# Performance work log

Measured on AMD Instinct MI355X. Metric: run time of the kernel, lower is better.

Reference implementation:

```python
import jax, jax.numpy as jnp
import numpy as np

S = 4096      # sequence length
E = 256       # embedding_dim
H = 256       # hidden_dim // 2 (per direction)
T = 16        # tagset size
V = 100000    # vocab size
START = 14
STOP = 15
NEG = -10000.0


def setup_inputs() -> dict:
    key = jax.random.key(0)
    ks = jax.random.split(key, 16)
    trans = jax.random.normal(ks[12], (T, T), jnp.float32)
    trans = trans.at[START, :].set(NEG).at[:, STOP].set(NEG)
    return {
        "sentence": jax.random.randint(ks[0], (S,), 0, V),
        "embed": jax.random.normal(ks[1], (V, E), jnp.float32),
        "W_ih_f": jax.random.normal(ks[2], (4 * H, E), jnp.float32) * 0.05,
        "W_hh_f": jax.random.normal(ks[3], (4 * H, H), jnp.float32) * 0.05,
        "b_ih_f": jax.random.normal(ks[4], (4 * H,), jnp.float32) * 0.05,
        "b_hh_f": jax.random.normal(ks[5], (4 * H,), jnp.float32) * 0.05,
        "W_ih_b": jax.random.normal(ks[6], (4 * H, E), jnp.float32) * 0.05,
        "W_hh_b": jax.random.normal(ks[7], (4 * H, H), jnp.float32) * 0.05,
        "b_ih_b": jax.random.normal(ks[8], (4 * H,), jnp.float32) * 0.05,
        "b_hh_b": jax.random.normal(ks[9], (4 * H,), jnp.float32) * 0.05,
        "W_out": jax.random.normal(ks[10], (T, 2 * H), jnp.float32) * 0.05,
        "b_out": jax.random.normal(ks[11], (T,), jnp.float32) * 0.05,
        "transitions": trans,
        "h0": jax.random.normal(ks[13], (2, H), jnp.float32),
        "c0": jax.random.normal(ks[14], (2, H), jnp.float32),
    }


def _lstm(x, h0, c0, W_ih, W_hh, b_ih, b_hh):
    """Single-direction LSTM over x:[S,E]; PyTorch gate order i,f,g,o."""
    b = b_ih + b_hh
    xg = x @ W_ih.T + b  # [S, 4H] precompute input contribution

    def step(carry, xt):
        h, c = carry
        g = xt + h @ W_hh.T
        i, f, gg, o = jnp.split(g, 4)
        i = jax.nn.sigmoid(i)
        f = jax.nn.sigmoid(f)
        gg = jnp.tanh(gg)
        o = jax.nn.sigmoid(o)
        c = f * c + i * gg
        h = o * jnp.tanh(c)
        return (h, c), h

    _, hs = jax.lax.scan(step, (h0, c0), xg)
    return hs  # [S, H]


def reference(sentence, embed, W_ih_f, W_hh_f, b_ih_f, b_hh_f,
              W_ih_b, W_hh_b, b_ih_b, b_hh_b, W_out, b_out,
              transitions, h0, c0):
    x = embed[sentence]  # [S, E]
    hf = _lstm(x, h0[0], c0[0], W_ih_f, W_hh_f, b_ih_f, b_hh_f)
    hb = _lstm(x[::-1], h0[1], c0[1], W_ih_b, W_hh_b, b_ih_b, b_hh_b)[::-1]
    feats = jnp.concatenate([hf, hb], axis=-1) @ W_out.T + b_out  # [S, T]

    # CRF forward algorithm (log partition). transitions[i, j] = score j -> i.
    alpha0 = jnp.full((T,), NEG, feats.dtype).at[START].set(0.0)

    def crf_step(alpha, emit):
        a = jax.nn.logsumexp(alpha[None, :] + transitions, axis=1) + emit
        return a, None

    alpha, _ = jax.lax.scan(crf_step, alpha0, feats)
    return jax.nn.logsumexp(alpha + transitions[STOP])
```

## Files before the change

kernel.cpp:

```cpp
#include <hip/hip_runtime.h>
#include <hip/hip_bf16.h>

#define S 4096
#define E 256
#define HH 256
#define TT 16
#define NEG_ -10000.0f
#define START_ 14
#define STOP_ 15

__device__ __forceinline__ float fast_exp(float x) {
    return __builtin_amdgcn_exp2f(x * 1.4426950408889634f);
}
__device__ __forceinline__ float fast_log(float x) {
    return 0.6931471805599453f * __builtin_amdgcn_logf(x);
}

__global__ __launch_bounds__(64) void quant4_kernel(
    const float* __restrict__ Wf, const float* __restrict__ Wb,
    const float* __restrict__ h0,
    int* __restrict__ wq4, float* __restrict__ wscale,
    int* __restrict__ hq0p, float* __restrict__ sh0)
{
    int blk = blockIdx.x, lane = threadIdx.x;
    const float* src;
    int* dst;
    float* scl;
    if (blk < 2048) {
        int d = blk >> 10, r = blk & 1023;
        src = (d == 0 ? Wf : Wb) + (size_t)r * 256;
        dst = wq4 + ((size_t)(d * 1024 + r)) * 32;
        scl = wscale + (d * 1024 + r);
    } else {
        int d = blk - 2048;
        src = h0 + (size_t)d * 256;
        dst = hq0p + d * 32;
        scl = sh0 + d;
    }
    float4 a = make_float4(0.f, 0.f, 0.f, 0.f), b = a;
    if (lane < 32) {
        a = ((const float4*)src)[2 * lane];
        b = ((const float4*)src)[2 * lane + 1];
    }
    float f[8] = {a.x, a.y, a.z, a.w, b.x, b.y, b.z, b.w};
    float m = 0.f;
    #pragma unroll
    for (int k = 0; k < 8; ++k) m = fmaxf(m, fabsf(f[k]));
    #pragma unroll
    for (int off = 1; off < 64; off <<= 1) m = fmaxf(m, __shfl_xor(m, off, 64));
    m = fmaxf(m, 1e-20f);
    float inv = 7.0f / m;
    if (lane < 32) {
        int dw = 0;
        #pragma unroll
        for (int k = 0; k < 8; ++k) {
            int q = __float2int_rn(f[k] * inv);
            q = max(-8, min(7, q));
            dw |= (q & 0xF) << (4 * k);
        }
        dst[lane] = dw;
    }
    if (lane == 0) *scl = m / 7.0f;
}

__global__ __launch_bounds__(256) void xg_kernel(
    const int* __restrict__ sent, const float* __restrict__ embed,
    const float* __restrict__ Wf, const float* __restrict__ bihf, const float* __restrict__ bhhf,
    const float* __restrict__ Wb, const float* __restrict__ bihb, const float* __restrict__ bhhb,
    float* __restrict__ xg)
{
    const int dir = blockIdx.y;
    const int t0 = blockIdx.x * 16;
    const int tid = threadIdx.x;
    const float* W = dir ? Wb : Wf;
    __shared__ float xt[16][256];
    for (int tt = 0; tt < 16; ++tt) {
        int t = t0 + tt;
        int pos = dir ? (S - 1 - t) : t;
        int w = sent[pos];
        xt[tt][tid] = embed[(size_t)w * 256 + tid];
    }
    __syncthreads();
    float acc[4][16];
    #pragma unroll
    for (int rc = 0; rc < 4; ++rc)
        #pragma unroll
        for (int tt = 0; tt < 16; ++tt) acc[rc][tt] = 0.f;
    for (int e = 0; e < 256; ++e) {
        float xv[16];
        #pragma unroll
        for (int tt = 0; tt < 16; ++tt) xv[tt] = xt[tt][e];
        #pragma unroll
        for (int rc = 0; rc < 4; ++rc) {
            float w = W[(size_t)(rc * 256 + tid) * 256 + e];
            #pragma unroll
            for (int tt = 0; tt < 16; ++tt) acc[rc][tt] += w * xv[tt];
        }
    }
    const float* bih = dir ? bihb : bihf;
    const float* bhh = dir ? bhhb : bhhf;
    float b0 = bih[0 * 256 + tid] + bhh[0 * 256 + tid];
    float b1 = bih[1 * 256 + tid] + bhh[1 * 256 + tid];
    float b2 = bih[2 * 256 + tid] + bhh[2 * 256 + tid];
    float b3 = bih[3 * 256 + tid] + bhh[3 * 256 + tid];
    #pragma unroll
    for (int tt = 0; tt < 16; ++tt) {
        float4 v;
        v.x = acc[0][tt] + b0;
        v.y = acc[1][tt] + b1;
        v.z = acc[2][tt] + b2;
        v.w = acc[3][tt] + b3;
        ((float4*)(xg + ((size_t)dir * S + (t0 + tt)) * 1024))[tid] = v;
    }
}

#define D8(a,w,h) "v_dot8_i32_i4 " a ", " w ", " h ", " a "\n\t"
#define CHK(h0,h1,h2,h3, a0,a1,a2,a3, b0,b1,b2,b3) \
  D8("v128",a0,h0) D8("v130",b0,h0) D8("v129",a1,h1) D8("v131",b1,h1) \
  D8("v128",a2,h2) D8("v130",b2,h2) D8("v129",a3,h3) D8("v131",b3,h3)

#define LSTM_BODY(XA0, XA1, BPAIR) \
  "global_load_dwordx2 " BPAIR ", v136, %[sxg]\n\t" \
  "ds_read_b128 v[96:99],   v138\n\t" \
  "ds_read_b128 v[100:103], v138 offset:16\n\t" \
  "ds_read_b128 v[104:107], v138 offset:32\n\t" \
  "ds_read_b128 v[108:111], v138 offset:48\n\t" \
  "ds_read_b128 v[112:115], v138 offset:64\n\t" \
  "ds_read_b128 v[116:119], v138 offset:80\n\t" \
  "ds_read_b128 v[120:123], v138 offset:96\n\t" \
  "ds_read_b128 v[124:127], v138 offset:112\n\t" \
  "v_mov_b32 v128, 0\n\t" \
  "v_mov_b32 v129, 0\n\t" \
  "v_mov_b32 v130, 0\n\t" \
  "v_mov_b32 v131, 0\n\t" \
  "s_waitcnt lgkmcnt(6)\n\t" \
  CHK("v96","v97","v98","v99",     "v32","v33","v34","v35", "v64","v65","v66","v67") \
  CHK("v100","v101","v102","v103", "v36","v37","v38","v39", "v68","v69","v70","v71") \
  "s_waitcnt lgkmcnt(4)\n\t" \
  CHK("v104","v105","v106","v107", "v40","v41","v42","v43", "v72","v73","v74","v75") \
  CHK("v108","v109","v110","v111", "v44","v45","v46","v47", "v76","v77","v78","v79") \
  "s_waitcnt lgkmcnt(2)\n\t" \
  CHK("v112","v113","v114","v115", "v48","v49","v50","v51", "v80","v81","v82","v83") \
  CHK("v116","v117","v118","v119", "v52","v53","v54","v55", "v84","v85","v86","v87") \
  "s_waitcnt lgkmcnt(0)\n\t" \
  CHK("v120","v121","v122","v123", "v56","v57","v58","v59", "v88","v89","v90","v91") \
  CHK("v124","v125","v126","v127", "v60","v61","v62","v63", "v92","v93","v94","v95") \
  "v_add_u32 v128, v128, v129\n\t" \
  "v_add_u32 v130, v130, v131\n\t" \
  "v_cvt_f32_i32 v140, v128\n\t" \
  "v_cvt_f32_i32 v141, v130\n\t" \
  "s_waitcnt vmcnt(2)\n\t" \
  "v_fma_f32 v142, v151, v140, " XA0 "\n\t" \
  "v_fma_f32 v143, v152, v141, " XA1 "\n\t" \
  "v_mov_b32 v151, %[s1f]\n\t" \
  "v_mov_b32 v152, %[s2f]\n\t" \
  "v_med3_f32 v142, v142, %[ncl], %[pcl]\n\t" \
  "v_mul_f32 v140, %[kk1], v142\n\t" \
  "v_mul_f32 v144, %[nk], v143\n\t" \
  "v_exp_f32 v140, v140\n\t" \
  "v_exp_f32 v144, v144\n\t" \
  "s_nop 1\n\t" \
  "v_fma_f32 v141, v140, %[mk], %[bk]\n\t" \
  "v_add_f32 v142, 1.0, v140\n\t" \
  "v_add_f32 v145, 1.0, v144\n\t" \
  "v_rcp_f32 v142, v142\n\t" \
  "v_rcp_f32 v145, v145\n\t" \
  "s_nop 1\n\t" \
  "v_mul_f32 v146, v141, v142\n\t" \
  "s_nop 1\n\t" \
  "v_mov_b32_dpp v147, v146 quad_perm:[1,0,3,2] row_mask:0xf bank_mask:0xf\n\t" \
  "v_mov_b32_dpp v148, v145 quad_perm:[1,0,3,2] row_mask:0xf bank_mask:0xf\n\t" \
  "v_cndmask_b32 v140, v146, v147, %[pm]\n\t" \
  "v_cndmask_b32 v141, v145, v148, %[pm]\n\t" \
  "v_cndmask_b32 v142, v147, v146, %[pm]\n\t" \
  "v_cndmask_b32 v143, v148, v145, %[pm]\n\t" \
  "v_mul_f32 v150, v141, v150\n\t" \
  "v_fmac_f32 v150, v140, v142\n\t" \
  "v_med3_f32 v140, v150, %[ncl], %[pcl]\n\t" \
  "v_mul_f32 v140, %[k2], v140\n\t" \
  "v_exp_f32 v140, v140\n\t" \
  "s_nop 1\n\t" \
  "v_add_f32 v141, -1.0, v140\n\t" \
  "v_add_f32 v142, 1.0, v140\n\t" \
  "v_rcp_f32 v142, v142\n\t" \
  "s_nop 1\n\t" \
  "v_mul_f32 v141, v141, v142\n\t" \
  "v_mul_f32 v144, v143, v141\n\t" \
  "global_store_dword v137, v144, %[shs]\n\t" \
  "v_mul_f32 v140, %[c7], v144\n\t" \
  "v_rndne_f32 v140, v140\n\t" \
  "v_cvt_i32_f32 v140, v140\n\t" \
  "v_and_b32 v140, 15, v140\n\t" \
  "s_nop 1\n\t" \
  "v_mov_b32_dpp v141, v140 quad_perm:[2,3,0,1] row_mask:0xf bank_mask:0xf\n\t" \
  "v_lshlrev_b32 v141, 4, v141\n\t" \
  "v_or_b32 v140, v140, v141\n\t" \
  "ds_write_b8 v139, v140\n\t" \
  "v_add_u32 v136, 0x1000, v136\n\t" \
  "v_add_u32 v137, 0x400, v137\n\t" \
  "v_xor_b32 v138, 0x80, v138\n\t" \
  "v_xor_b32 v139, 0x80, v139\n\t" \
  "s_waitcnt lgkmcnt(0)\n\t" \
  "s_barrier\n\t"

__global__ __launch_bounds__(512, 2) void lstm_kernel(
    const float* __restrict__ xg, const int* __restrict__ wq4,
    const float* __restrict__ wscale, const int* __restrict__ hq0p,
    const float* __restrict__ sh0, const float* __restrict__ c0,
    float* __restrict__ hs)
{
    const int d = blockIdx.x;
    const int t = threadIdx.x;
    const int m = t >> 1;
    const int odd = t & 1;
    const int r1 = odd * 512 + m;
    const int r2 = r1 + 256;

    __shared__ alignas(16) int hq4buf[128];

    const int*   wq_d = wq4 + (size_t)d * 32768;
    const float* xg_d = xg + (size_t)d * S * 1024;
    float*       hs_d = hs + (size_t)d * S * 256;
    const float s1 = wscale[d * 1024 + r1];
    const float s2 = wscale[d * 1024 + r2];
    const float sh0v = sh0[d];
    const float c0v = c0[d * 256 + m];
    const int h0v = hq0p[d * 32 + (t & 31)];
    const unsigned h0a  = (unsigned)(t & 31) * 4u;
    const unsigned xoff = (unsigned)t * 8u;
    const unsigned hoff = (unsigned)m * 4u;
    const unsigned voA  = (unsigned)r1 * 128u;
    const unsigned voB  = (unsigned)r2 * 128u;
    const unsigned waddr = ((t & 3) == 0) ? (128u + (unsigned)(t >> 2))
                                          : (256u + (unsigned)(t & 63));
    const float sc1i = s1 * sh0v, sc2i = s2 * sh0v;
    const float sc1f = s1 * (1.0f / 7.0f);
    const float sc2f = s2 * (1.0f / 7.0f);
    const float kk1 = odd ? 2.8853900817779268f : -1.4426950408889634f;
    const float mkv = odd ? 1.0f : 0.0f;
    const float bkv = odd ? -1.0f : 1.0f;
    const float nkv = -1.4426950408889634f;
    const float k2v = 2.8853900817779268f;
    const float c7 = 7.0f;
    const float nclv = -30.0f, pclv = 30.0f;
    const unsigned long long pmask = 0xAAAAAAAAAAAAAAAAULL;
    const unsigned lds_keep = (unsigned)(size_t)&hq4buf[0];
    int cnt = S / 2;

    asm volatile(
        "v_mov_b32 v136, %[xoff]\n\t"
        "v_mov_b32 v137, %[hoff]\n\t"
        "v_mov_b32 v138, 0\n\t"
        "v_mov_b32 v139, %[wad]\n\t"
        "v_mov_b32 v150, %[c0v]\n\t"
        "v_mov_b32 v151, %[s1i]\n\t"
        "v_mov_b32 v152, %[s2i]\n\t"
        "ds_write_b32 %[h0a], %[h0v]\n\t"
        "global_load_dwordx4 v[32:35], %[voA], %[swq]\n\t"
        "global_load_dwordx4 v[36:39], %[voA], %[swq] offset:16\n\t"
        "global_load_dwordx4 v[40:43], %[voA], %[swq] offset:32\n\t"
        "global_load_dwordx4 v[44:47], %[voA], %[swq] offset:48\n\t"
        "global_load_dwordx4 v[48:51], %[voA], %[swq] offset:64\n\t"
        "global_load_dwordx4 v[52:55], %[voA], %[swq] offset:80\n\t"
        "global_load_dwordx4 v[56:59], %[voA], %[swq] offset:96\n\t"
        "global_load_dwordx4 v[60:63], %[voA], %[swq] offset:112\n\t"
        "global_load_dwordx4 v[64:67], %[voB], %[swq]\n\t"
        "global_load_dwordx4 v[68:71], %[voB], %[swq] offset:16\n\t"
        "global_load_dwordx4 v[72:75], %[voB], %[swq] offset:32\n\t"
        "global_load_dwordx4 v[76:79], %[voB], %[swq] offset:48\n\t"
        "global_load_dwordx4 v[80:83], %[voB], %[swq] offset:64\n\t"
        "global_load_dwordx4 v[84:87], %[voB], %[swq] offset:80\n\t"
        "global_load_dwordx4 v[88:91], %[voB], %[swq] offset:96\n\t"
        "global_load_dwordx4 v[92:95], %[voB], %[swq] offset:112\n\t"
        "global_load_dwordx2 v[132:133], v136, %[sxg]\n\t"
        "v_add_u32 v136, 0x1000, v136\n\t"
        "s_waitcnt vmcnt(0) lgkmcnt(0)\n\t"
        "s_barrier\n\t"
        "Llstm%=:\n\t"
        LSTM_BODY("v132", "v133", "v[134:135]")
        LSTM_BODY("v134", "v135", "v[132:133]")
        "s_add_i32 %[cnt], %[cnt], -1\n\t"
        "s_cmp_lg_u32 %[cnt], 0\n\t"
        "s_cbranch_scc1 Llstm%=\n\t"
        : [cnt] "+s"(cnt)
        : [sxg] "s"(xg_d), [shs] "s"(hs_d), [swq] "s"(wq_d), [pm] "s"(pmask),
          [xoff] "v"(xoff), [hoff] "v"(hoff), [wad] "v"(waddr), [c0v] "v"(c0v),
          [s1i] "v"(sc1i), [s2i] "v"(sc2i), [s1f] "v"(sc1f), [s2f] "v"(sc2f),
          [kk1] "v"(kk1), [mk] "v"(mkv), [bk] "v"(bkv), [nk] "v"(nkv),
          [k2] "v"(k2v), [c7] "v"(c7), [ncl] "v"(nclv), [pcl] "v"(pclv),
          [voA] "v"(voA), [voB] "v"(voB), [h0a] "v"(h0a), [h0v] "v"(h0v),
          [keep] "v"(lds_keep)
        : "memory", "scc",
          "v32","v33","v34","v35","v36","v37","v38","v39",
          "v40","v41","v42","v43","v44","v45","v46","v47",
          "v48","v49","v50","v51","v52","v53","v54","v55",
          "v56","v57","v58","v59","v60","v61","v62","v63",
          "v64","v65","v66","v67","v68","v69","v70","v71",
          "v72","v73","v74","v75","v76","v77","v78","v79",
          "v80","v81","v82","v83","v84","v85","v86","v87",
          "v88","v89","v90","v91","v92","v93","v94","v95",
          "v96","v97","v98","v99","v100","v101","v102","v103",
          "v104","v105","v106","v107","v108","v109","v110","v111",
          "v112","v113","v114","v115","v116","v117","v118","v119",
          "v120","v121","v122","v123","v124","v125","v126","v127",
          "v128","v129","v130","v131","v132","v133","v134","v135",
          "v136","v137","v138","v139","v140","v141","v142","v143",
          "v144","v145","v146","v147","v148","v149","v150","v151","v152");
}

__global__ __launch_bounds__(256) void feats_kernel(
    const float* __restrict__ hs, const float* __restrict__ Wout,
    const float* __restrict__ bout, float* __restrict__ feats)
{
    __shared__ float Wl[16][513];
    int tid = threadIdx.x;
    for (int i = tid; i < 16 * 512; i += 256) Wl[i >> 9][i & 511] = Wout[i];
    __syncthreads();
    int tt = tid >> 4, tag = tid & 15;
    int tcur = blockIdx.x * 16 + tt;
    const float* hf = hs + (size_t)tcur * 256;
    const float* hb = hs + (size_t)S * 256 + (size_t)(S - 1 - tcur) * 256;
    float acc = bout[tag];
    for (int k = 0; k < 256; ++k) acc += Wl[tag][k] * hf[k];
    for (int k = 0; k < 256; ++k) acc += Wl[tag][256 + k] * hb[k];
    feats[(size_t)tcur * 16 + tag] = acc;
}

__global__ __launch_bounds__(256) void crf_chunk_kernel(
    const float* __restrict__ feats, const float* __restrict__ trans,
    float* __restrict__ P)
{
    int chunk = blockIdx.x;
    int tid = threadIdx.x;
    int i = tid >> 4, jj = tid & 15;
    __shared__ float Mt[2][16][17];
    float tr[16];
    #pragma unroll
    for (int k = 0; k < 16; ++k) tr[k] = trans[i * 16 + k];
    int t0 = chunk * 64;
    float emit = feats[(size_t)t0 * 16 + i];
    Mt[0][jj][i] = tr[jj] + emit;
    __syncthreads();
    int cur = 0;
    float em_next = feats[(size_t)(t0 + 1) * 16 + i];
    for (int s = 1; s < 64; ++s) {
        float em = em_next;
        if (s + 1 < 64) em_next = feats[(size_t)(t0 + s + 1) * 16 + i];
        float v[16];
        #pragma unroll
        for (int k = 0; k < 16; ++k) v[k] = tr[k] + Mt[cur][jj][k];
        float m = v[0];
        #pragma unroll
        for (int k = 1; k < 16; ++k) m = fmaxf(m, v[k]);
        float ssum = 0.f;
        #pragma unroll
        for (int k = 0; k < 16; ++k) ssum += fast_exp(v[k] - m);
        float nv = em + m + fast_log(ssum);
        Mt[cur ^ 1][jj][i] = nv;
        cur ^= 1;
        __syncthreads();
    }
    P[((size_t)chunk * 16 + i) * 16 + jj] = Mt[cur][jj][i];
}

__global__ __launch_bounds__(256) void crf_fold_kernel(
    const float* __restrict__ P, const float* __restrict__ trans,
    float* __restrict__ out)
{
    int tid = threadIdx.x;
    int i = tid >> 4, jj = tid & 15;
    __shared__ float alpha[16];
    if (tid < 16) alpha[tid] = (tid == START_) ? 0.0f : NEG_;
    __syncthreads();
    for (int cc = 0; cc < 64; ++cc) {
        float pv = P[((size_t)cc * 16 + i) * 16 + jj];
        float v = pv + alpha[jj];
        float m = v;
        #pragma unroll
        for (int off = 1; off < 16; off <<= 1) m = fmaxf(m, __shfl_xor(m, off, 64));
        float e = fast_exp(v - m);
        #pragma unroll
        for (int off = 1; off < 16; off <<= 1) e += __shfl_xor(e, off, 64);
        float nv = m + fast_log(e);
        __syncthreads();
        if (jj == 0) alpha[i] = nv;
        __syncthreads();
    }
    if (tid < 16) {
        float v = alpha[tid] + trans[STOP_ * 16 + tid];
        float m = v;
        #pragma unroll
        for (int off = 1; off < 16; off <<= 1) m = fmaxf(m, __shfl_xor(m, off, 64));
        float e = fast_exp(v - m);
        #pragma unroll
        for (int off = 1; off < 16; off <<= 1) e += __shfl_xor(e, off, 64);
        if (tid == 0) out[0] = m + fast_log(e);
    }
}

extern "C" void kernel_launch(void* const* d_in, const int* in_sizes, int n_in,
                              void* d_out, int out_size, void* d_ws, size_t ws_size,
                              hipStream_t stream) {
    const int*   sent  = (const int*)d_in[0];
    const float* embed = (const float*)d_in[1];
    const float* Wihf  = (const float*)d_in[2];
    const float* Whhf  = (const float*)d_in[3];
    const float* bihf  = (const float*)d_in[4];
    const float* bhhf  = (const float*)d_in[5];
    const float* Wihb  = (const float*)d_in[6];
    const float* Whhb  = (const float*)d_in[7];
    const float* bihb  = (const float*)d_in[8];
    const float* bhhb  = (const float*)d_in[9];
    const float* Wout  = (const float*)d_in[10];
    const float* bout  = (const float*)d_in[11];
    const float* trans = (const float*)d_in[12];
    const float* h0    = (const float*)d_in[13];
    const float* c0    = (const float*)d_in[14];
    float* out = (float*)d_out;

    char* ws = (char*)d_ws;
    constexpr size_t OFF_XG     = 0;
    constexpr size_t OFF_WQ     = OFF_XG + (size_t)2 * S * 1024 * 4;
    constexpr size_t OFF_WSCALE = OFF_WQ + (size_t)2 * 1024 * 32 * 4;
    constexpr size_t OFF_HQ0    = OFF_WSCALE + 2 * 1024 * 4;
    constexpr size_t OFF_SH0    = OFF_HQ0 + 2 * 32 * 4;
    constexpr size_t OFF_HS     = OFF_SH0 + 256;
    constexpr size_t OFF_FEATS  = OFF_HS + (size_t)2 * S * 256 * 4;
    constexpr size_t OFF_P      = OFF_FEATS + (size_t)S * 16 * 4;

    float* xg     = (float*)(ws + OFF_XG);
    int*   wq4    = (int*)(ws + OFF_WQ);
    float* wscale = (float*)(ws + OFF_WSCALE);
    int*   hq0p   = (int*)(ws + OFF_HQ0);
    float* sh0    = (float*)(ws + OFF_SH0);
    float* hs     = (float*)(ws + OFF_HS);
    float* feats  = (float*)(ws + OFF_FEATS);
    float* P      = (float*)(ws + OFF_P);

    quant4_kernel<<<dim3(2050), dim3(64), 0, stream>>>(Whhf, Whhb, h0, wq4, wscale, hq0p, sh0);
    xg_kernel<<<dim3(256, 2), dim3(256), 0, stream>>>(sent, embed, Wihf, bihf, bhhf,
                                                      Wihb, bihb, bhhb, xg);
    lstm_kernel<<<dim3(2), dim3(512), 0, stream>>>(xg, wq4, wscale, hq0p, sh0, c0, hs);
    feats_kernel<<<dim3(256), dim3(256), 0, stream>>>(hs, Wout, bout, feats);
    crf_chunk_kernel<<<dim3(64), dim3(256), 0, stream>>>(feats, trans, P);
    crf_fold_kernel<<<dim3(1), dim3(256), 0, stream>>>(P, trans, out);
}
```

Before: 2.613 ms.

## Split LSTM recurrence to one gate row per thread with 1024-thread blocks

The recurrent LSTM kernel now uses 1024 threads per direction, each thread owning a single gate row instead of two. This halves the per-thread int4 dot-product chain and register footprint, and gates are exchanged across the quad with DPP moves. Non-leader lanes write their h outputs to a dump buffer so the store path needs no branch. The initial hidden state is quantized with a fixed scale so the first step matches the steady-state scaling. The cost is more waves synchronizing at each per-step barrier and some redundant lane work.

```diff
diff --git a/kernel.cpp b/kernel.cpp
--- a/kernel.cpp
+++ b/kernel.cpp
@@ -26,6 +26,7 @@
     const float* src;
     int* dst;
     float* scl;
+    bool fixed = false;
     if (blk < 2048) {
         int d = blk >> 10, r = blk & 1023;
         src = (d == 0 ? Wf : Wb) + (size_t)r * 256;
@@ -36,6 +37,7 @@
         src = h0 + (size_t)d * 256;
         dst = hq0p + d * 32;
         scl = sh0 + d;
+        fixed = true;
     }
     float4 a = make_float4(0.f, 0.f, 0.f, 0.f), b = a;
     if (lane < 32) {
@@ -49,7 +51,7 @@
     #pragma unroll
     for (int off = 1; off < 64; off <<= 1) m = fmaxf(m, __shfl_xor(m, off, 64));
     m = fmaxf(m, 1e-20f);
-    float inv = 7.0f / m;
+    float inv = fixed ? 7.0f : (7.0f / m);
     if (lane < 32) {
         int dw = 0;
         #pragma unroll
@@ -60,7 +62,7 @@
         }
         dst[lane] = dw;
     }
-    if (lane == 0) *scl = m / 7.0f;
+    if (lane == 0) *scl = fixed ? (1.0f / 7.0f) : (m / 7.0f);
 }
 
 __global__ __launch_bounds__(256) void xg_kernel(
@@ -115,181 +117,148 @@
 }
 
 #define D8(a,w,h) "v_dot8_i32_i4 " a ", " w ", " h ", " a "\n\t"
-#define CHK(h0,h1,h2,h3, a0,a1,a2,a3, b0,b1,b2,b3) \
-  D8("v128",a0,h0) D8("v130",b0,h0) D8("v129",a1,h1) D8("v131",b1,h1) \
-  D8("v128",a2,h2) D8("v130",b2,h2) D8("v129",a3,h3) D8("v131",b3,h3)
-
-#define LSTM_BODY(XA0, XA1, BPAIR) \
-  "global_load_dwordx2 " BPAIR ", v136, %[sxg]\n\t" \
-  "ds_read_b128 v[96:99],   v138\n\t" \
-  "ds_read_b128 v[100:103], v138 offset:16\n\t" \
-  "ds_read_b128 v[104:107], v138 offset:32\n\t" \
-  "ds_read_b128 v[108:111], v138 offset:48\n\t" \
-  "ds_read_b128 v[112:115], v138 offset:64\n\t" \
-  "ds_read_b128 v[116:119], v138 offset:80\n\t" \
-  "ds_read_b128 v[120:123], v138 offset:96\n\t" \
-  "ds_read_b128 v[124:127], v138 offset:112\n\t" \
-  "v_mov_b32 v128, 0\n\t" \
-  "v_mov_b32 v129, 0\n\t" \
-  "v_mov_b32 v130, 0\n\t" \
-  "v_mov_b32 v131, 0\n\t" \
+
+#define LSTM_BODY(XA, XN) \
+  "global_load_dword " XN ", v100, %[sxg]\n\t" \
+  "ds_read_b128 v[64:67], v102\n\t" \
+  "ds_read_b128 v[68:71], v102 offset:16\n\t" \
+  "ds_read_b128 v[72:75], v102 offset:32\n\t" \
+  "ds_read_b128 v[76:79], v102 offset:48\n\t" \
+  "ds_read_b128 v[80:83], v102 offset:64\n\t" \
+  "ds_read_b128 v[84:87], v102 offset:80\n\t" \
+  "ds_read_b128 v[88:91], v102 offset:96\n\t" \
+  "ds_read_b128 v[92:95], v102 offset:112\n\t" \
+  "v_mov_b32 v96, 0\n\t" \
+  "v_mov_b32 v97, 0\n\t" \
   "s_waitcnt lgkmcnt(6)\n\t" \
-  CHK("v96","v97","v98","v99",     "v32","v33","v34","v35", "v64","v65","v66","v67") \
-  CHK("v100","v101","v102","v103", "v36","v37","v38","v39", "v68","v69","v70","v71") \
+  D8("v96","v32","v64") D8("v97","v33","v65") D8("v96","v34","v66") D8("v97","v35","v67") \
+  D8("v96","v36","v68") D8("v97","v37","v69") D8("v96","v38","v70") D8("v97","v39","v71") \
   "s_waitcnt lgkmcnt(4)\n\t" \
-  CHK("v104","v105","v106","v107", "v40","v41","v42","v43", "v72","v73","v74","v75") \
-  CHK("v108","v109","v110","v111", "v44","v45","v46","v47", "v76","v77","v78","v79") \
+  D8("v96","v40","v72") D8("v97","v41","v73") D8("v96","v42","v74") D8("v97","v43","v75") \
+  D8("v96","v44","v76") D8("v97","v45","v77") D8("v96","v46","v78") D8("v97","v47","v79") \
   "s_waitcnt lgkmcnt(2)\n\t" \
-  CHK("v112","v113","v114","v115", "v48","v49","v50","v51", "v80","v81","v82","v83") \
-  CHK("v116","v117","v118","v119", "v52","v53","v54","v55", "v84","v85","v86","v87") \
+  D8("v96","v48","v80") D8("v97","v49","v81") D8("v96","v50","v82") D8("v97","v51","v83") \
+  D8("v96","v52","v84") D8("v97","v53","v85") D8("v96","v54","v86") D8("v97","v55","v87") \
   "s_waitcnt lgkmcnt(0)\n\t" \
-  CHK("v120","v121","v122","v123", "v56","v57","v58","v59", "v88","v89","v90","v91") \
-  CHK("v124","v125","v126","v127", "v60","v61","v62","v63", "v92","v93","v94","v95") \
-  "v_add_u32 v128, v128, v129\n\t" \
-  "v_add_u32 v130, v130, v131\n\t" \
-  "v_cvt_f32_i32 v140, v128\n\t" \
-  "v_cvt_f32_i32 v141, v130\n\t" \
+  D8("v96","v56","v88") D8("v97","v57","v89") D8("v96","v58","v90") D8("v97","v59","v91") \
+  D8("v96","v60","v92") D8("v97","v61","v93") D8("v96","v62","v94") D8("v97","v63","v95") \
+  "v_add_u32 v96, v96, v97\n\t" \
+  "v_cvt_f32_i32 v104, v96\n\t" \
   "s_waitcnt vmcnt(2)\n\t" \
-  "v_fma_f32 v142, v151, v140, " XA0 "\n\t" \
-  "v_fma_f32 v143, v152, v141, " XA1 "\n\t" \
-  "v_mov_b32 v151, %[s1f]\n\t" \
-  "v_mov_b32 v152, %[s2f]\n\t" \
-  "v_med3_f32 v142, v142, %[ncl], %[pcl]\n\t" \
-  "v_mul_f32 v140, %[kk1], v142\n\t" \
-  "v_mul_f32 v144, %[nk], v143\n\t" \
-  "v_exp_f32 v140, v140\n\t" \
-  "v_exp_f32 v144, v144\n\t" \
+  "v_fma_f32 v105, %[sc], v104, " XA "\n\t" \
+  "v_med3_f32 v105, v105, %[ncl], %[pcl]\n\t" \
+  "v_mul_f32 v104, %[kk], v105\n\t" \
+  "v_exp_f32 v104, v104\n\t" \
   "s_nop 1\n\t" \
-  "v_fma_f32 v141, v140, %[mk], %[bk]\n\t" \
-  "v_add_f32 v142, 1.0, v140\n\t" \
-  "v_add_f32 v145, 1.0, v144\n\t" \
-  "v_rcp_f32 v142, v142\n\t" \
-  "v_rcp_f32 v145, v145\n\t" \
+  "v_fma_f32 v106, v104, %[mk], %[bk]\n\t" \
+  "v_add_f32 v107, 1.0, v104\n\t" \
+  "v_rcp_f32 v107, v107\n\t" \
   "s_nop 1\n\t" \
-  "v_mul_f32 v146, v141, v142\n\t" \
+  "v_mul_f32 v108, v106, v107\n\t" \
   "s_nop 1\n\t" \
-  "v_mov_b32_dpp v147, v146 quad_perm:[1,0,3,2] row_mask:0xf bank_mask:0xf\n\t" \
-  "v_mov_b32_dpp v148, v145 quad_perm:[1,0,3,2] row_mask:0xf bank_mask:0xf\n\t" \
-  "v_cndmask_b32 v140, v146, v147, %[pm]\n\t" \
-  "v_cndmask_b32 v141, v145, v148, %[pm]\n\t" \
-  "v_cndmask_b32 v142, v147, v146, %[pm]\n\t" \
-  "v_cndmask_b32 v143, v148, v145, %[pm]\n\t" \
-  "v_mul_f32 v150, v141, v150\n\t" \
-  "v_fmac_f32 v150, v140, v142\n\t" \
-  "v_med3_f32 v140, v150, %[ncl], %[pcl]\n\t" \
-  "v_mul_f32 v140, %[k2], v140\n\t" \
-  "v_exp_f32 v140, v140\n\t" \
+  "v_mov_b32_dpp v109, v108 quad_perm:[1,0,3,2] row_mask:0xf bank_mask:0xf\n\t" \
+  "v_mov_b32_dpp v110, v108 quad_perm:[2,3,0,1] row_mask:0xf bank_mask:0xf\n\t" \
+  "v_mov_b32_dpp v111, v108 quad_perm:[3,2,1,0] row_mask:0xf bank_mask:0xf\n\t" \
+  "v_mul_f32 v114, v109, v114\n\t" \
+  "v_fmac_f32 v114, v108, v110\n\t" \
+  "v_med3_f32 v104, v114, %[ncl], %[pcl]\n\t" \
+  "v_mul_f32 v104, %[k2], v104\n\t" \
+  "v_exp_f32 v104, v104\n\t" \
   "s_nop 1\n\t" \
-  "v_add_f32 v141, -1.0, v140\n\t" \
-  "v_add_f32 v142, 1.0, v140\n\t" \
-  "v_rcp_f32 v142, v142\n\t" \
+  "v_add_f32 v106, -1.0, v104\n\t" \
+  "v_add_f32 v107, 1.0, v104\n\t" \
+  "v_rcp_f32 v107, v107\n\t" \
   "s_nop 1\n\t" \
-  "v_mul_f32 v141, v141, v142\n\t" \
-  "v_mul_f32 v144, v143, v141\n\t" \
-  "global_store_dword v137, v144, %[shs]\n\t" \
-  "v_mul_f32 v140, %[c7], v144\n\t" \
-  "v_rndne_f32 v140, v140\n\t" \
-  "v_cvt_i32_f32 v140, v140\n\t" \
-  "v_and_b32 v140, 15, v140\n\t" \
-  "s_nop 1\n\t" \
-  "v_mov_b32_dpp v141, v140 quad_perm:[2,3,0,1] row_mask:0xf bank_mask:0xf\n\t" \
-  "v_lshlrev_b32 v141, 4, v141\n\t" \
-  "v_or_b32 v140, v140, v141\n\t" \
-  "ds_write_b8 v139, v140\n\t" \
-  "v_add_u32 v136, 0x1000, v136\n\t" \
-  "v_add_u32 v137, 0x400, v137\n\t" \
-  "v_xor_b32 v138, 0x80, v138\n\t" \
-  "v_xor_b32 v139, 0x80, v139\n\t" \
+  "v_mul_f32 v106, v106, v107\n\t" \
+  "v_mul_f32 v112, v111, v106\n\t" \
+  "global_store_dword v101, v112, %[shs]\n\t" \
+  "v_mul_f32 v104, %[c7], v112\n\t" \
+  "v_rndne_f32 v104, v104\n\t" \
+  "v_cvt_i32_f32 v104, v104\n\t" \
+  "v_and_b32 v104, 15, v104\n\t" \
+  "ds_swizzle_b32 v105, v104 offset:0x101F\n\t" \
+  "s_waitcnt lgkmcnt(0)\n\t" \
+  "v_lshlrev_b32 v105, 4, v105\n\t" \
+  "v_or_b32 v104, v104, v105\n\t" \
+  "ds_write_b8 v103, v104\n\t" \
+  "v_add_u32 v100, 0x1000, v100\n\t" \
+  "v_add_u32 v101, v113, v101\n\t" \
+  "v_xor_b32 v102, 0x80, v102\n\t" \
+  "v_xor_b32 v103, 0x80, v103\n\t" \
   "s_waitcnt lgkmcnt(0)\n\t" \
   "s_barrier\n\t"
 
-__global__ __launch_bounds__(512, 2) void lstm_kernel(
+__global__ __launch_bounds__(1024, 4) void lstm_kernel(
     const float* __restrict__ xg, const int* __restrict__ wq4,
     const float* __restrict__ wscale, const int* __restrict__ hq0p,
-    const float* __restrict__ sh0, const float* __restrict__ c0,
-    float* __restrict__ hs)
+    const float* __restrict__ c0, float* __restrict__ hs,
+    unsigned dump_off_bytes)
 {
     const int d = blockIdx.x;
     const int t = threadIdx.x;
-    const int m = t >> 1;
-    const int odd = t & 1;
-    const int r1 = odd * 512 + m;
-    const int r2 = r1 + 256;
+    const int m = t >> 2;
+    const int g = t & 3;
+    const int r = g * 256 + m;
 
     __shared__ alignas(16) int hq4buf[128];
 
     const int*   wq_d = wq4 + (size_t)d * 32768;
     const float* xg_d = xg + (size_t)d * S * 1024;
     float*       hs_d = hs + (size_t)d * S * 256;
-    const float s1 = wscale[d * 1024 + r1];
-    const float s2 = wscale[d * 1024 + r2];
-    const float sh0v = sh0[d];
+    const float sc  = wscale[d * 1024 + r] * (1.0f / 7.0f);
     const float c0v = c0[d * 256 + m];
     const int h0v = hq0p[d * 32 + (t & 31)];
-    const unsigned h0a  = (unsigned)(t & 31) * 4u;
-    const unsigned xoff = (unsigned)t * 8u;
-    const unsigned hoff = (unsigned)m * 4u;
-    const unsigned voA  = (unsigned)r1 * 128u;
-    const unsigned voB  = (unsigned)r2 * 128u;
-    const unsigned waddr = ((t & 3) == 0) ? (128u + (unsigned)(t >> 2))
-                                          : (256u + (unsigned)(t & 63));
-    const float sc1i = s1 * sh0v, sc2i = s2 * sh0v;
-    const float sc1f = s1 * (1.0f / 7.0f);
-    const float sc2f = s2 * (1.0f / 7.0f);
-    const float kk1 = odd ? 2.8853900817779268f : -1.4426950408889634f;
-    const float mkv = odd ? 1.0f : 0.0f;
-    const float bkv = odd ? -1.0f : 1.0f;
-    const float nkv = -1.4426950408889634f;
-    const float k2v = 2.8853900817779268f;
+    const unsigned h0a = (t < 32) ? (unsigned)t * 4u : (256u + (unsigned)(t & 63) * 4u);
+    const unsigned xai = (unsigned)t * 4u;
+    const bool leader = (g == 0);
+    const unsigned dump_rel = dump_off_bytes - (unsigned)((size_t)d * S * 256 * 4);
+    const unsigned hsi = leader ? (unsigned)m * 4u : (dump_rel + (unsigned)(t & 255) * 4u);
+    const unsigned dlt = leader ? 1024u : 0u;
+    const unsigned hwi = ((t & 7) == 0) ? (128u + (unsigned)(t >> 3))
+                                        : (256u + (unsigned)(t & 63) * 4u);
+    const unsigned voW = (unsigned)r * 128u;
+    const float kk = (g == 2) ? 2.8853900817779268f : -1.4426950408889634f;
+    const float mk = (g == 2) ? 1.0f : 0.0f;
+    const float bk = (g == 2) ? -1.0f : 1.0f;
+    const float k2 = 2.8853900817779268f;
     const float c7 = 7.0f;
-    const float nclv = -30.0f, pclv = 30.0f;
-    const unsigned long long pmask = 0xAAAAAAAAAAAAAAAAULL;
+    const float ncl = -30.0f, pcl = 30.0f;
     const unsigned lds_keep = (unsigned)(size_t)&hq4buf[0];
     int cnt = S / 2;
 
     asm volatile(
-        "v_mov_b32 v136, %[xoff]\n\t"
-        "v_mov_b32 v137, %[hoff]\n\t"
-        "v_mov_b32 v138, 0\n\t"
-        "v_mov_b32 v139, %[wad]\n\t"
-        "v_mov_b32 v150, %[c0v]\n\t"
-        "v_mov_b32 v151, %[s1i]\n\t"
-        "v_mov_b32 v152, %[s2i]\n\t"
+        "v_mov_b32 v100, %[xai]\n\t"
+        "v_mov_b32 v101, %[hsi]\n\t"
+        "v_mov_b32 v102, 0\n\t"
+        "v_mov_b32 v103, %[hwi]\n\t"
+        "v_mov_b32 v113, %[dlt]\n\t"
+        "v_mov_b32 v114, %[c0v]\n\t"
         "ds_write_b32 %[h0a], %[h0v]\n\t"
-        "global_load_dwordx4 v[32:35], %[voA], %[swq]\n\t"
-        "global_load_dwordx4 v[36:39], %[voA], %[swq] offset:16\n\t"
-        "global_load_dwordx4 v[40:43], %[voA], %[swq] offset:32\n\t"
-        "global_load_dwordx4 v[44:47], %[voA], %[swq] offset:48\n\t"
-        "global_load_dwordx4 v[48:51], %[voA], %[swq] offset:64\n\t"
-        "global_load_dwordx4 v[52:55], %[voA], %[swq] offset:80\n\t"
-        "global_load_dwordx4 v[56:59], %[voA], %[swq] offset:96\n\t"
-        "global_load_dwordx4 v[60:63], %[voA], %[swq] offset:112\n\t"
-        "global_load_dwordx4 v[64:67], %[voB], %[swq]\n\t"
-        "global_load_dwordx4 v[68:71], %[voB], %[swq] offset:16\n\t"
-        "global_load_dwordx4 v[72:75], %[voB], %[swq] offset:32\n\t"
-        "global_load_dwordx4 v[76:79], %[voB], %[swq] offset:48\n\t"
-        "global_load_dwordx4 v[80:83], %[voB], %[swq] offset:64\n\t"
-        "global_load_dwordx4 v[84:87], %[voB], %[swq] offset:80\n\t"
-        "global_load_dwordx4 v[88:91], %[voB], %[swq] offset:96\n\t"
-        "global_load_dwordx4 v[92:95], %[voB], %[swq] offset:112\n\t"
-        "global_load_dwordx2 v[132:133], v136, %[sxg]\n\t"
-        "v_add_u32 v136, 0x1000, v136\n\t"
+        "global_load_dwordx4 v[32:35], %[voW], %[swq]\n\t"
+        "global_load_dwordx4 v[36:39], %[voW], %[swq] offset:16\n\t"
+        "global_load_dwordx4 v[40:43], %[voW], %[swq] offset:32\n\t"
+        "global_load_dwordx4 v[44:47], %[voW], %[swq] offset:48\n\t"
+        "global_load_dwordx4 v[48:51], %[voW], %[swq] offset:64\n\t"
+        "global_load_dwordx4 v[52:55], %[voW], %[swq] offset:80\n\t"
+        "global_load_dwordx4 v[56:59], %[voW], %[swq] offset:96\n\t"
+        "global_load_dwordx4 v[60:63], %[voW], %[swq] offset:112\n\t"
+        "global_load_dword v98, v100, %[sxg]\n\t"
+        "v_add_u32 v100, 0x1000, v100\n\t"
         "s_waitcnt vmcnt(0) lgkmcnt(0)\n\t"
         "s_barrier\n\t"
         "Llstm%=:\n\t"
-        LSTM_BODY("v132", "v133", "v[134:135]")
-        LSTM_BODY("v134", "v135", "v[132:133]")
+        LSTM_BODY("v98", "v99")
+        LSTM_BODY("v99", "v98")
         "s_add_i32 %[cnt], %[cnt], -1\n\t"
         "s_cmp_lg_u32 %[cnt], 0\n\t"
         "s_cbranch_scc1 Llstm%=\n\t"
         : [cnt] "+s"(cnt)
-        : [sxg] "s"(xg_d), [shs] "s"(hs_d), [swq] "s"(wq_d), [pm] "s"(pmask),
-          [xoff] "v"(xoff), [hoff] "v"(hoff), [wad] "v"(waddr), [c0v] "v"(c0v),
-          [s1i] "v"(sc1i), [s2i] "v"(sc2i), [s1f] "v"(sc1f), [s2f] "v"(sc2f),
-          [kk1] "v"(kk1), [mk] "v"(mkv), [bk] "v"(bkv), [nk] "v"(nkv),
-          [k2] "v"(k2v), [c7] "v"(c7), [ncl] "v"(nclv), [pcl] "v"(pclv),
-          [voA] "v"(voA), [voB] "v"(voB), [h0a] "v"(h0a), [h0v] "v"(h0v),
-          [keep] "v"(lds_keep)
+        : [sxg] "s"(xg_d), [shs] "s"(hs_d), [swq] "s"(wq_d),
+          [xai] "v"(xai), [hsi] "v"(hsi), [hwi] "v"(hwi), [dlt] "v"(dlt),
+          [c0v] "v"(c0v), [h0a] "v"(h0a), [h0v] "v"(h0v),
+          [sc] "v"(sc), [kk] "v"(kk), [mk] "v"(mk), [bk] "v"(bk),
+          [k2] "v"(k2), [c7] "v"(c7), [ncl] "v"(ncl), [pcl] "v"(pcl),
+          [voW] "v"(voW), [keep] "v"(lds_keep)
         : "memory", "scc",
           "v32","v33","v34","v35","v36","v37","v38","v39",
           "v40","v41","v42","v43","v44","v45","v46","v47",
@@ -301,11 +270,7 @@
           "v88","v89","v90","v91","v92","v93","v94","v95",
           "v96","v97","v98","v99","v100","v101","v102","v103",
           "v104","v105","v106","v107","v108","v109","v110","v111",
-          "v112","v113","v114","v115","v116","v117","v118","v119",
-          "v120","v121","v122","v123","v124","v125","v126","v127",
-          "v128","v129","v130","v131","v132","v133","v134","v135",
-          "v136","v137","v138","v139","v140","v141","v142","v143",
-          "v144","v145","v146","v147","v148","v149","v150","v151","v152");
+          "v112","v113","v114");
 }
 
 __global__ __launch_bounds__(256) void feats_kernel(
@@ -425,7 +390,8 @@
     constexpr size_t OFF_HQ0    = OFF_WSCALE + 2 * 1024 * 4;
     constexpr size_t OFF_SH0    = OFF_HQ0 + 2 * 32 * 4;
     constexpr size_t OFF_HS     = OFF_SH0 + 256;
-    constexpr size_t OFF_FEATS  = OFF_HS + (size_t)2 * S * 256 * 4;
+    constexpr size_t OFF_DUMP   = OFF_HS + (size_t)2 * S * 256 * 4;
+    constexpr size_t OFF_FEATS  = OFF_DUMP + 4096;
     constexpr size_t OFF_P      = OFF_FEATS + (size_t)S * 16 * 4;
 
     float* xg     = (float*)(ws + OFF_XG);
@@ -436,11 +402,12 @@
     float* hs     = (float*)(ws + OFF_HS);
     float* feats  = (float*)(ws + OFF_FEATS);
     float* P      = (float*)(ws + OFF_P);
+    const unsigned dump_off = (unsigned)(OFF_DUMP - OFF_HS);
 
     quant4_kernel<<<dim3(2050), dim3(64), 0, stream>>>(Whhf, Whhb, h0, wq4, wscale, hq0p, sh0);
     xg_kernel<<<dim3(256, 2), dim3(256), 0, stream>>>(sent, embed, Wihf, bihf, bhhf,
                                                       Wihb, bihb, bhhb, xg);
-    lstm_kernel<<<dim3(2), dim3(512), 0, stream>>>(xg, wq4, wscale, hq0p, sh0, c0, hs);
+    lstm_kernel<<<dim3(2), dim3(1024), 0, stream>>>(xg, wq4, wscale, hq0p, c0, hs, dump_off);
     feats_kernel<<<dim3(256), dim3(256), 0, stream>>>(hs, Wout, bout, feats);
     crf_chunk_kernel<<<dim3(64), dim3(256), 0, stream>>>(feats, trans, P);
     crf_fold_kernel<<<dim3(1), dim3(256), 0, stream>>>(P, trans, out);
```

Result: slower. 2.953 ms (+13.0%).
